# Optimization experiments

Measured on AMD Instinct MI355X. Metric: run time of the kernel, lower is better.

## Reference

```python
import jax, jax.numpy as jnp
import numpy as np

# ---- constants derived from MyTestNetwork.__init__ ----
PARTICLE_RADIUS = 0.025
RADIUS_SCALE = 1.5
EXTENT = RADIUS_SCALE * 6.0 * PARTICLE_RADIUS   # 0.225 (filter_extent)
RADIUS = EXTENT / 2.0                            # 0.1125 (search radius)
KS = 4                                           # kernel_size per dim
C_IN, C_OUT = 3, 32                              # vel channels -> layer_channels[0]
N_IN = 8192
N_OUT = 8192
E_PAD = 600000                                   # padded flat edge count
EPS = 1e-12
FOUR_OVER_PI = 4.0 / np.pi


def setup_inputs() -> dict:
    key = jax.random.key(0)
    k1, k2, k3, k4, k5 = jax.random.split(key, 5)
    pos0 = jax.random.uniform(k1, (N_IN, 3), jnp.float32)   # fluid positions
    pos1 = jax.random.uniform(k2, (N_OUT, 3), jnp.float32)  # output positions
    vel = jax.random.uniform(k3, (N_IN, 3), jnp.float32)    # input features
    W = jax.random.normal(k4, (KS, KS, KS, C_IN, C_OUT), jnp.float32) * 0.1
    b = jax.random.normal(k5, (C_OUT,), jnp.float32) * 0.01
    # ---- radius neighbor search (setup-time, numpy, chunked brute force) ----
    p0 = np.asarray(pos0)
    p1 = np.asarray(pos1)
    r2 = RADIUS * RADIUS
    src_l, dst_l = [], []
    for s in range(0, N_OUT, 1024):
        d2 = ((p1[s:s + 1024, None, :] - p0[None, :, :]) ** 2).sum(-1)
        dd, ss = np.nonzero((d2 < r2) & (d2 > 0.0))  # >0: ignore_query_points
        dst_l.append((dd + s).astype(np.int32))
        src_l.append(ss.astype(np.int32))
    src = np.concatenate(src_l)
    dst = np.concatenate(dst_l)
    E = min(len(src), E_PAD)
    src_p = np.zeros(E_PAD, np.int32)
    dst_p = np.zeros(E_PAD, np.int32)
    mask = np.zeros(E_PAD, np.float32)
    src_p[:E] = src[:E]
    dst_p[:E] = dst[:E]
    mask[:E] = 1.0
    return {"vel": vel, "pos0": pos0, "pos1": pos1, "W": W, "b": b,
            "src": jnp.asarray(src_p), "dst": jnp.asarray(dst_p),
            "edge_mask": jnp.asarray(mask)}


def _ball_to_cube_volume_preserving(rel):
    """Maps points in the unit ball to the unit cube [-1,1]^3 (Open3D mapping)."""
    x, y, z = rel[:, 0], rel[:, 1], rel[:, 2]
    sq = x * x + y * y + z * z
    norm = jnp.sqrt(sq + EPS)
    # --- sphere -> cylinder ---
    top = 1.25 * z * z > (x * x + y * y)
    s_top = jnp.sqrt(3.0 * norm / (norm + jnp.abs(z) + EPS))
    s_side = norm / jnp.sqrt(x * x + y * y + EPS)
    cx = jnp.where(top, x * s_top, x * s_side)
    cy = jnp.where(top, y * s_top, y * s_side)
    cz = jnp.where(top, jnp.sign(z) * norm, 1.5 * z)
    zero = sq < 1e-12
    cx = jnp.where(zero, 0.0, cx)
    cy = jnp.where(zero, 0.0, cy)
    cz = jnp.where(zero, 0.0, cz)
    # --- cylinder -> cube (inverse Shirley-Chiu concentric map on xy) ---
    nxy = jnp.sqrt(cx * cx + cy * cy + EPS)
    xs = jnp.where(jnp.abs(cx) > EPS, cx, 1.0)
    ys = jnp.where(jnp.abs(cy) > EPS, cy, 1.0)
    ux1 = jnp.sign(cx) * nxy
    uy1 = jnp.sign(cx) * nxy * FOUR_OVER_PI * jnp.arctan(cy / xs)
    ux2 = jnp.sign(cy) * nxy * FOUR_OVER_PI * jnp.arctan(cx / ys)
    uy2 = jnp.sign(cy) * nxy
    c1 = cx * cx >= cy * cy
    ux = jnp.where(c1, ux1, ux2)
    uy = jnp.where(c1, uy1, uy2)
    zero_xy = (cx * cx + cy * cy) < 1e-12
    ux = jnp.where(zero_xy, 0.0, ux)
    uy = jnp.where(zero_xy, 0.0, uy)
    return jnp.stack([ux, uy, cz], axis=-1)


def _cconv(vel, pos0, pos1, W, b, src, dst, edge_mask):
    # relative neighbor positions, normalized so the search ball is the unit ball
    rel = (pos0[src] - pos1[dst]) / RADIUS              # (E,3)
    r_sqr = jnp.sum(rel * rel, axis=-1)                 # (E,)
    # poly6 window * validity mask (padded / out-of-ball edges contribute 0)
    win = jnp.clip((1.0 - r_sqr) ** 3, 0.0, 1.0) * (r_sqr < 1.0) * edge_mask
    cube = _ball_to_cube_volume_preserving(rel)         # (E,3) in [-1,1]^3
    grid = jnp.clip((cube + 1.0) * 0.5 * (KS - 1), 0.0, KS - 1)  # align_corners
    i0 = jnp.clip(jnp.floor(grid), 0, KS - 2).astype(jnp.int32)
    f = grid - i0
    ix, iy, iz = i0[:, 0], i0[:, 1], i0[:, 2]
    fx, fy, fz = f[:, 0], f[:, 1], f[:, 2]
    W2 = W.reshape(KS * KS * KS, C_IN, C_OUT)
    feat = vel[src]                                     # (E,3)
    msg = jnp.zeros((src.shape[0], C_OUT), vel.dtype)
    # trilinear interpolation over the 8 kernel-grid corners
    for dz in (0, 1):
        wz = fz if dz else (1.0 - fz)
        for dy in (0, 1):
            wy = fy if dy else (1.0 - fy)
            for dx in (0, 1):
                wx = fx if dx else (1.0 - fx)
                w = wz * wy * wx * win                  # (E,)
                idx = ((iz + dz) * KS + (iy + dy)) * KS + (ix + dx)
                msg = msg + w[:, None] * jnp.einsum('ec,eco->eo', feat, W2[idx])
    out = jax.ops.segment_sum(msg, dst, num_segments=N_OUT) + b
    return out


def reference(vel, pos0, pos1, W, b, src, dst, edge_mask):
    return _cconv(vel, pos0, pos1, W, b, src, dst, edge_mask)
```

## Files before the change

### kernel.cpp

```cpp
#include <hip/hip_runtime.h>
#include <math.h>

#define N_NODES 8192
#define C_OUT 32
constexpr float INV_RADIUS   = 1.0f / 0.1125f;
constexpr float EPS          = 1e-12f;
constexpr float FOUR_OVER_PI = 1.27323954473516f;

typedef __attribute__((ext_vector_type(8))) _Float16 half8;
typedef __attribute__((ext_vector_type(4))) float    floatx4;

__device__ __forceinline__ float frcp(float x)  { float r; asm("v_rcp_f32 %0, %1"  : "=v"(r) : "v"(x)); return r; }
__device__ __forceinline__ float frsq(float x)  { float r; asm("v_rsq_f32 %0, %1"  : "=v"(r) : "v"(x)); return r; }
__device__ __forceinline__ float fsqrt_(float x){ float r; asm("v_sqrt_f32 %0, %1" : "=v"(r) : "v"(x)); return r; }

__device__ __forceinline__ float sgnf(float v) {
    return (v > 0.f) ? 1.f : ((v < 0.f) ? -1.f : 0.f);
}

__device__ __forceinline__ unsigned pkh(float a, float b) {
    union { _Float16 h[2]; unsigned u; } x;
    x.h[0] = (_Float16)a; x.h[1] = (_Float16)b;
    return x.u;
}

__device__ __forceinline__ float atan01(float q) {
    float t = q * q;
    float p = fmaf(t, -0.01172120f, 0.05265332f);
    p = fmaf(t, p, -0.11643287f);
    p = fmaf(t, p,  0.19354346f);
    p = fmaf(t, p, -0.33262347f);
    p = fmaf(t, p,  0.99997726f);
    return q * p;
}

#define PV_OFF   0
#define ROFF_OFF 262144
#define W2H_OFF  294928

__global__ __launch_bounds__(256) void prep_kernel(
    const float* __restrict__ pos0,
    const float* __restrict__ vel,
    const float* __restrict__ W,
    const int*   __restrict__ dst,
    const float* __restrict__ mask,
    int E,
    int*   __restrict__ row_off,
    float* __restrict__ pv,
    _Float16* __restrict__ W2h)
{
    int tid = blockIdx.x * blockDim.x + threadIdx.x;

    if (tid < 6400) {
        int o = tid / 200, j = tid - o * 200;
        _Float16 val = (_Float16)0.f;
        if (j < 192) {
            int nc = j >> 4, m = j & 15;
            int iz = m >> 2, iy = m & 3, ix = nc / 3, c = nc - ix * 3;
            int cell = (iz * 4 + iy) * 4 + ix;
            val = (_Float16)W[(cell * 3 + c) * 32 + o];
        }
        W2h[tid] = val;
    }
    if (tid < N_NODES) {
        float4 p = make_float4(pos0[3*tid+0], pos0[3*tid+1], pos0[3*tid+2], 0.f);
        float4 v = make_float4(vel [3*tid+0], vel [3*tid+1], vel [3*tid+2], 0.f);
        ((float4*)pv)[2*tid+0] = p;
        ((float4*)pv)[2*tid+1] = v;
    }

    if (tid >= E) return;
    int kc_cur  = (mask[tid] != 0.f) ? min(dst[tid], N_NODES) : N_NODES;
    int kc_prev = -1;
    if (tid > 0)
        kc_prev = (mask[tid-1] != 0.f) ? min(dst[tid-1], N_NODES) : N_NODES;
    for (int n = kc_prev + 1; n <= kc_cur; ++n)
        row_off[n] = tid;
}

__global__ __launch_bounds__(512) void cconv_kernel(
    const float* __restrict__ pv,
    const float* __restrict__ pos1,
    const int*   __restrict__ src,
    const int*   __restrict__ row_off,
    const _Float16* __restrict__ W2h,
    const float* __restrict__ b,
    float* __restrict__ out)
{
    __shared__ float    Glds[8][64 * 18];
    __shared__ _Float16 A_lds[16][200];

    int t = threadIdx.x, wave = t >> 6, lane = t & 63;
    int q = lane >> 4, mr = lane & 15;
    int node = blockIdx.x * 8 + wave;

    floatx4 acc = {0.f, 0.f, 0.f, 0.f};

    float px = pos1[3*node+0], py = pos1[3*node+1], pz = pos1[3*node+2];
    int e0 = row_off[node], e1 = row_off[node+1];

    float* myrec = &Glds[wave][lane * 18];
    const _Float16* hp = (const _Float16*)&Glds[wave][0];

    for (int eb = e0; eb < e1; eb += 64) {
        int cnt = min(64, e1 - eb);
        bool valid = lane < cnt;
        int s = src[valid ? eb + lane : eb];
        float4 p = ((const float4*)pv)[2*s+0];
        float4 v = ((const float4*)pv)[2*s+1];

        float rx = (p.x - px) * INV_RADIUS;
        float ry = (p.y - py) * INV_RADIUS;
        float rz = (p.z - pz) * INV_RADIUS;
        float r2 = rx*rx + ry*ry + rz*rz;
        float om  = 1.f - r2;
        float win = om * om * om;
        if (!valid || r2 >= 1.f) win = 0.f;

        float x = rx, y = ry, z = rz;
        float ax2y2 = x*x + y*y;
        float norm  = fsqrt_(r2 + EPS);
        bool  top   = 1.25f * z * z > ax2y2;
        float s_top  = fsqrt_(3.f * norm * frcp(norm + fabsf(z) + EPS));
        float s_side = norm * frsq(ax2y2 + EPS);
        float sel = top ? s_top : s_side;
        float cx = x * sel;
        float cy = y * sel;
        float cz = top ? sgnf(z) * norm : 1.5f * z;
        bool zero = r2 < 1e-12f;
        cx = zero ? 0.f : cx;  cy = zero ? 0.f : cy;  cz = zero ? 0.f : cz;

        float cx2 = cx*cx, cy2 = cy*cy;
        float nxy = fsqrt_(cx2 + cy2 + EPS);
        bool  c1  = cx2 >= cy2;
        float xs  = (fabsf(cx) > EPS) ? cx : 1.f;
        float ys  = (fabsf(cy) > EPS) ? cy : 1.f;
        float num = c1 ? cy : cx;
        float den = c1 ? xs : ys;
        float at  = atan01(num * frcp(den)) * FOUR_OVER_PI * nxy;
        float scx = sgnf(cx), scy = sgnf(cy);
        float ux = c1 ? scx * nxy : scy * at;
        float uy = c1 ? scx * at  : scy * nxy;
        bool zxy = (cx2 + cy2) < 1e-12f;
        ux = zxy ? 0.f : ux;  uy = zxy ? 0.f : uy;

        float gx = fminf(fmaxf((ux + 1.f) * 1.5f, 0.f), 3.f);
        float gy = fminf(fmaxf((uy + 1.f) * 1.5f, 0.f), 3.f);
        float gz = fminf(fmaxf((cz + 1.f) * 1.5f, 0.f), 3.f);

        float wvx = win * v.x, wvy = win * v.y, wvz = win * v.z;

        float hx0 = fmaxf(1.f - fabsf(gx - 0.f), 0.f);
        float hx1 = fmaxf(1.f - fabsf(gx - 1.f), 0.f);
        float hx2 = fmaxf(1.f - fabsf(gx - 2.f), 0.f);
        float hx3 = fmaxf(1.f - fabsf(gx - 3.f), 0.f);
        float hy0 = fmaxf(1.f - fabsf(gy - 0.f), 0.f);
        float hy1 = fmaxf(1.f - fabsf(gy - 1.f), 0.f);
        float hy2 = fmaxf(1.f - fabsf(gy - 2.f), 0.f);
        float hy3 = fmaxf(1.f - fabsf(gy - 3.f), 0.f);
        float hz0 = fmaxf(1.f - fabsf(gz - 0.f), 0.f);
        float hz1 = fmaxf(1.f - fabsf(gz - 1.f), 0.f);
        float hz2 = fmaxf(1.f - fabsf(gz - 2.f), 0.f);
        float hz3 = fmaxf(1.f - fabsf(gz - 3.f), 0.f);

        unsigned A0 = pkh(hz0*hy0, hz0*hy1), A1 = pkh(hz0*hy2, hz0*hy3);
        unsigned A2 = pkh(hz1*hy0, hz1*hy1), A3 = pkh(hz1*hy2, hz1*hy3);
        unsigned A4 = pkh(hz2*hy0, hz2*hy1), A5 = pkh(hz2*hy2, hz2*hy3);
        unsigned A6 = pkh(hz3*hy0, hz3*hy1), A7 = pkh(hz3*hy2, hz3*hy3);
        unsigned B0 = pkh(hx0*wvx, hx0*wvy), B1 = pkh(hx0*wvz, hx1*wvx);
        unsigned B2 = pkh(hx1*wvy, hx1*wvz), B3 = pkh(hx2*wvx, hx2*wvy);
        unsigned B4 = pkh(hx2*wvz, hx3*wvx), B5 = pkh(hx3*wvy, hx3*wvz);

        float2* wp = (float2*)myrec;
        wp[0] = make_float2(__uint_as_float(A0), __uint_as_float(A1));
        wp[1] = make_float2(__uint_as_float(A2), __uint_as_float(A3));
        wp[2] = make_float2(__uint_as_float(A4), __uint_as_float(A5));
        wp[3] = make_float2(__uint_as_float(A6), __uint_as_float(A7));
        wp[4] = make_float2(__uint_as_float(B0), __uint_as_float(B1));
        wp[5] = make_float2(__uint_as_float(B2), __uint_as_float(B3));
        wp[6] = make_float2(__uint_as_float(B4), __uint_as_float(B5));
        wp[7] = make_float2(0.f, 0.f);

        int nkk = (cnt > 32) ? 2 : 1;
        for (int kk = 0; kk < nkk; ++kk) {
            union { _Float16 h[8]; half8 v8; } fa, fb;
            #pragma unroll
            for (int i = 0; i < 8; ++i) {
                int rec = kk * 32 + q * 8 + i;
                fa.h[i] = hp[rec * 36 + mr];
                fb.h[i] = hp[rec * 36 + 16 + mr];
            }
            acc = __builtin_amdgcn_mfma_f32_16x16x32_f16(fa.v8, fb.v8, acc, 0, 0, 0);
        }
    }

    if (mr < 12) {
        uint2 u = make_uint2(pkh(acc[0], acc[1]), pkh(acc[2], acc[3]));
        *(uint2*)&A_lds[wave][mr * 16 + 4 * q] = u;
    }
    __syncthreads();

    if (wave == 0) {
        floatx4 o0 = {0.f, 0.f, 0.f, 0.f};
        floatx4 o1 = {0.f, 0.f, 0.f, 0.f};
        #pragma unroll
        for (int kk = 0; kk < 6; ++kk) {
            half8 af = *(const half8*)&A_lds[mr][kk * 32 + q * 8];
            half8 b0 = *(const half8*)&W2h[mr * 200 + kk * 32 + q * 8];
            half8 b1 = *(const half8*)&W2h[(16 + mr) * 200 + kk * 32 + q * 8];
            o0 = __builtin_amdgcn_mfma_f32_16x16x32_f16(af, b0, o0, 0, 0, 0);
            o1 = __builtin_amdgcn_mfma_f32_16x16x32_f16(af, b1, o1, 0, 0, 0);
        }
        if (q < 2) {
            int n0 = blockIdx.x * 8;
            float bv0 = b[mr], bv1 = b[16 + mr];
            #pragma unroll
            for (int r = 0; r < 4; ++r) {
                int nd = n0 + 4 * q + r;
                out[nd * C_OUT + mr]      = o0[r] + bv0;
                out[nd * C_OUT + 16 + mr] = o1[r] + bv1;
            }
        }
    }
}

extern "C" void kernel_launch(void* const* d_in, const int* in_sizes, int n_in,
                              void* d_out, int out_size, void* d_ws, size_t ws_size,
                              hipStream_t stream)
{
    const float* vel  = (const float*)d_in[0];
    const float* pos0 = (const float*)d_in[1];
    const float* pos1 = (const float*)d_in[2];
    const float* W    = (const float*)d_in[3];
    const float* b    = (const float*)d_in[4];
    const int*   src  = (const int*)d_in[5];
    const int*   dst  = (const int*)d_in[6];
    const float* mask = (const float*)d_in[7];
    int E = in_sizes[5];

    char* ws = (char*)d_ws;
    float*    pv      = (float*)(ws + PV_OFF);
    int*      row_off = (int*)  (ws + ROFF_OFF);
    _Float16* W2h     = (_Float16*)(ws + W2H_OFF);

    prep_kernel<<<(E + 255) / 256, 256, 0, stream>>>(pos0, vel, W, dst, mask, E, row_off, pv, W2h);
    cconv_kernel<<<N_NODES / 8, 512, 0, stream>>>(pv, pos1, src, row_off, W2h, b, (float*)d_out);
}
```

Baseline: 17.40 us.

## Vectorize row-offset build and drop block-wide sync in output GEMM

The prep kernel now handles four edges per thread with int4/float4 loads, launching a quarter of the threads for the CSR row-offset construction. The cconv epilogue no longer gathers all eight waves' accumulators into shared memory behind a __syncthreads for wave 0 to multiply. Each wave now runs its own small MFMA product against the weights using its Glds slice and writes only row 0 of the result. This removes the block barrier and the serial single-wave epilogue, at the cost of seven-eighths of the output-GEMM MFMA rows being wasted per wave. The prep grid size assumes E is a multiple of 4 (E_PAD=600000 is), and the node-count and weight-prep threshold checks still need enough threads.

```diff
diff --git a/kernel.cpp b/kernel.cpp
--- a/kernel.cpp
+++ b/kernel.cpp
@@ -69,13 +69,21 @@
         ((float4*)pv)[2*tid+1] = v;
     }
 
-    if (tid >= E) return;
-    int kc_cur  = (mask[tid] != 0.f) ? min(dst[tid], N_NODES) : N_NODES;
-    int kc_prev = -1;
-    if (tid > 0)
-        kc_prev = (mask[tid-1] != 0.f) ? min(dst[tid-1], N_NODES) : N_NODES;
-    for (int n = kc_prev + 1; n <= kc_cur; ++n)
-        row_off[n] = tid;
+    int e0i = tid * 4;
+    if (e0i >= E) return;
+    int4   d4 = ((const int4*)dst)[tid];
+    float4 m4 = ((const float4*)mask)[tid];
+    int kcs[5];
+    kcs[0] = (e0i == 0) ? -1
+           : ((mask[e0i-1] != 0.f) ? min(dst[e0i-1], N_NODES) : N_NODES);
+    kcs[1] = (m4.x != 0.f) ? min(d4.x, N_NODES) : N_NODES;
+    kcs[2] = (m4.y != 0.f) ? min(d4.y, N_NODES) : N_NODES;
+    kcs[3] = (m4.z != 0.f) ? min(d4.z, N_NODES) : N_NODES;
+    kcs[4] = (m4.w != 0.f) ? min(d4.w, N_NODES) : N_NODES;
+    #pragma unroll
+    for (int i = 0; i < 4; ++i)
+        for (int n = kcs[i] + 1; n <= kcs[i+1]; ++n)
+            row_off[n] = e0i + i;
 }
 
 __global__ __launch_bounds__(512) void cconv_kernel(
@@ -87,8 +95,7 @@
     const float* __restrict__ b,
     float* __restrict__ out)
 {
-    __shared__ float    Glds[8][64 * 18];
-    __shared__ _Float16 A_lds[16][200];
+    __shared__ float Glds[8][64 * 18];
 
     int t = threadIdx.x, wave = t >> 6, lane = t & 63;
     int q = lane >> 4, mr = lane & 15;
@@ -194,33 +201,25 @@
         }
     }
 
+    _Float16* Gw = (_Float16*)&Glds[wave][0];
     if (mr < 12) {
         uint2 u = make_uint2(pkh(acc[0], acc[1]), pkh(acc[2], acc[3]));
-        *(uint2*)&A_lds[wave][mr * 16 + 4 * q] = u;
-    }
-    __syncthreads();
-
-    if (wave == 0) {
-        floatx4 o0 = {0.f, 0.f, 0.f, 0.f};
-        floatx4 o1 = {0.f, 0.f, 0.f, 0.f};
-        #pragma unroll
-        for (int kk = 0; kk < 6; ++kk) {
-            half8 af = *(const half8*)&A_lds[mr][kk * 32 + q * 8];
-            half8 b0 = *(const half8*)&W2h[mr * 200 + kk * 32 + q * 8];
-            half8 b1 = *(const half8*)&W2h[(16 + mr) * 200 + kk * 32 + q * 8];
-            o0 = __builtin_amdgcn_mfma_f32_16x16x32_f16(af, b0, o0, 0, 0, 0);
-            o1 = __builtin_amdgcn_mfma_f32_16x16x32_f16(af, b1, o1, 0, 0, 0);
-        }
-        if (q < 2) {
-            int n0 = blockIdx.x * 8;
-            float bv0 = b[mr], bv1 = b[16 + mr];
-            #pragma unroll
-            for (int r = 0; r < 4; ++r) {
-                int nd = n0 + 4 * q + r;
-                out[nd * C_OUT + mr]      = o0[r] + bv0;
-                out[nd * C_OUT + 16 + mr] = o1[r] + bv1;
-            }
-        }
+        *(uint2*)&Gw[mr * 16 + 4 * q] = u;
+    }
+
+    floatx4 o0 = {0.f, 0.f, 0.f, 0.f};
+    floatx4 o1 = {0.f, 0.f, 0.f, 0.f};
+    #pragma unroll
+    for (int kk = 0; kk < 6; ++kk) {
+        half8 af = *(const half8*)&Gw[kk * 32 + q * 8];
+        half8 b0 = *(const half8*)&W2h[mr * 200 + kk * 32 + q * 8];
+        half8 b1 = *(const half8*)&W2h[(16 + mr) * 200 + kk * 32 + q * 8];
+        o0 = __builtin_amdgcn_mfma_f32_16x16x32_f16(af, b0, o0, 0, 0, 0);
+        o1 = __builtin_amdgcn_mfma_f32_16x16x32_f16(af, b1, o1, 0, 0, 0);
+    }
+    if (q == 0) {
+        out[node * C_OUT + mr]      = o0[0] + b[mr];
+        out[node * C_OUT + 16 + mr] = o1[0] + b[16 + mr];
     }
 }
 
@@ -243,6 +242,6 @@
     int*      row_off = (int*)  (ws + ROFF_OFF);
     _Float16* W2h     = (_Float16*)(ws + W2H_OFF);
 
-    prep_kernel<<<(E + 255) / 256, 256, 0, stream>>>(pos0, vel, W, dst, mask, E, row_off, pv, W2h);
+    prep_kernel<<<(E / 4 + 255) / 256, 256, 0, stream>>>(pos0, vel, W, dst, mask, E, row_off, pv, W2h);
     cconv_kernel<<<N_NODES / 8, 512, 0, stream>>>(pv, pos1, src, row_off, W2h, b, (float*)d_out);
 }
```

Measured after the change: 19.93 us. 14.6% more time.
